# Kernel optimization log

Hardware: AMD Instinct MI355X
Metric: run time of the kernel (lower is better)

## Reference

```python
import jax, jax.numpy as jnp
import numpy as np

EPS = 1e-08

def setup_inputs() -> dict:
    key = jax.random.key(0)
    k1, k2, k3, k4 = jax.random.split(key, 4)
    B, T, D, D_sample = 16, 512, 2048, 4096
    z_hist = jax.random.normal(k1, (B, T, D), dtype=jnp.float32)
    decay_rates = jax.random.normal(k2, (D_sample,), dtype=jnp.float32)
    idx_i = jax.random.randint(k3, (D_sample,), 0, D)
    idx_j = jax.random.randint(k4, (D_sample,), 0, D)
    return {"z_hist": z_hist, "decay_rates": decay_rates, "idx_i": idx_i, "idx_j": idx_j}

def reference(z_hist, decay_rates, idx_i, idx_j):
    B, T, D = z_hist.shape
    r = jax.nn.softplus(decay_rates)                      # [N]
    times = jnp.arange(T, dtype=z_hist.dtype)             # [T]
    # decay[t, n] = exp(-r_n * (T - 1 - t))
    decay = jnp.exp(-r[None, :] * (T - 1 - times)[:, None])  # [T, N]
    z_i = z_hist[:, :, idx_i]                              # [B, T, N]
    z_j = z_hist[:, :, idx_j]                              # [B, T, N]
    num = jnp.einsum('btn,btn,tn->bn', z_i, z_j, decay)    # [B, N]
    den = jnp.sqrt(decay.sum(axis=0) + EPS)                # [N]
    return num / den[None, :]
```

## Files before the change

kernel.cpp:

```cpp
#include <hip/hip_runtime.h>
#include <hip/hip_bf16.h>
#include <math.h>

#define B_   16
#define T_   512
#define D_   2048
#define DS_  4096
#define TCHUNK 4
#define EPS_ 1e-8f


__global__ __launch_bounds__(256) void pre_kernel(const float* __restrict__ decay_rates,
                                                  float* __restrict__ num,
                                                  float* __restrict__ inv_den,
                                                  float* __restrict__ neg_r,
                                                  float* __restrict__ er) {
    int gtid = blockIdx.x * 256 + threadIdx.x;
    num[gtid] = 0.f;
    if (gtid < DS_) {
        float x = decay_rates[gtid];
        float r = (x > 20.f) ? x : log1pf(expf(x));
        float S = expm1f(-r * (float)T_) / expm1f(-r);
        inv_den[gtid] = 1.0f / sqrtf(S + EPS_);
        neg_r[gtid]   = -r;
        er[gtid]      = expf(r);
    }
}

__global__ __launch_bounds__(256, 5) void main_kernel(const float* __restrict__ z,
                                                      const int* __restrict__ idx_i,
                                                      const int* __restrict__ idx_j,
                                                      const float* __restrict__ neg_r,
                                                      const float* __restrict__ er,
                                                      float* __restrict__ num) {
    __shared__ float4 quads[D_];
    const int tc  = blockIdx.x;
    const int b   = blockIdx.y;
    const int tid = threadIdx.x;
    const int t0  = tc * TCHUNK;
    const float* base = z + ((size_t)b * T_ + t0) * D_;

    #pragma unroll
    for (int it = 0; it < D_ / 256; ++it) {
        int c = tid + it * 256;
        quads[c] = make_float4(base[c], base[D_ + c], base[2 * D_ + c], base[3 * D_ + c]);
    }
    __syncthreads();

    const int kbase = (T_ - 1) - t0;

    #pragma unroll 1
    for (int s = 0; s < DS_ / 256; ++s) {
        const int n  = tid + s * 256;
        const int ii = idx_i[n];
        const int jj = idx_j[n];
        const float g = er[n];
        const float w0 = __expf(neg_r[n] * (float)kbase);
        float4 vi = quads[ii];
        float4 vj = quads[jj];
        float p0 = vi.x * vj.x;
        float p1 = vi.y * vj.y;
        float p2 = vi.z * vj.z;
        float p3 = vi.w * vj.w;
        float acc = w0 * (p0 + g * (p1 + g * (p2 + g * p3)));
        atomicAdd(&num[b * DS_ + n], acc);
    }
}

__global__ __launch_bounds__(256) void fin_kernel(const float* __restrict__ num,
                                                  const float* __restrict__ inv_den,
                                                  float* __restrict__ out) {
    int gtid = blockIdx.x * 256 + threadIdx.x;
    out[gtid] = num[gtid] * inv_den[gtid & (DS_ - 1)];
}

extern "C" void kernel_launch(void* const* d_in, const int* in_sizes, int n_in,
                              void* d_out, int out_size, void* d_ws, size_t ws_size,
                              hipStream_t stream) {
    const float* z  = (const float*)d_in[0];
    const float* dr = (const float*)d_in[1];
    const int*   ii = (const int*)d_in[2];
    const int*   jj = (const int*)d_in[3];
    float* out = (float*)d_out;

    float* num     = (float*)d_ws;
    float* inv_den = num + B_ * DS_;
    float* neg_r   = inv_den + DS_;
    float* er      = neg_r + DS_;

    hipLaunchKernelGGL(pre_kernel, dim3((B_ * DS_) / 256), dim3(256), 0, stream,
                       dr, num, inv_den, neg_r, er);
    hipLaunchKernelGGL(main_kernel, dim3(T_ / TCHUNK, B_), dim3(256), 0, stream,
                       z, ii, jj, neg_r, er, num);
    hipLaunchKernelGGL(fin_kernel, dim3((B_ * DS_) / 256), dim3(256), 0, stream,
                       num, inv_den, out);
}
```

Before: 135.4 us.

## Bucket samples by decay horizon and skip negligibly decayed time steps

A new single-block kernel buckets the sampled pairs by how many time steps their decay weight stays above roughly exp(-34.5). It stores per-bucket parameters in sorted order so warps get uniform skip decisions. The main kernel now handles two time chunks per block, keeps accumulators in registers, and updates the weight multiplicatively with a precomputed exp(-4r). It skips pairs whose decay is negligible and issues one atomic per pair per block. This cuts LDS gathers, exp evaluations and atomic traffic. It adds an extra launch and still loads the full z slab in every block.

```diff
diff --git a/kernel.cpp b/kernel.cpp
--- a/kernel.cpp
+++ b/kernel.cpp
@@ -1,70 +1,145 @@
 #include <hip/hip_runtime.h>
-#include <hip/hip_bf16.h>
 #include <math.h>
 
-#define B_   16
-#define T_   512
-#define D_   2048
-#define DS_  4096
+#define B_    16
+#define T_    512
+#define D_    2048
+#define DS_   4096
 #define TCHUNK 4
-#define EPS_ 1e-8f
+#define TCPB   2
+#define TSPLIT (T_ / (TCHUNK * TCPB))
+#define EPS_  1e-8f
+#define CLOG  34.5f
 
+
+__device__ __forceinline__ float softplus_f(float x) {
+    return (x > 20.f) ? x : log1pf(expf(x));
+}
 
 __global__ __launch_bounds__(256) void pre_kernel(const float* __restrict__ decay_rates,
                                                   float* __restrict__ num,
-                                                  float* __restrict__ inv_den,
-                                                  float* __restrict__ neg_r,
-                                                  float* __restrict__ er) {
+                                                  float* __restrict__ inv_den) {
     int gtid = blockIdx.x * 256 + threadIdx.x;
     num[gtid] = 0.f;
     if (gtid < DS_) {
-        float x = decay_rates[gtid];
-        float r = (x > 20.f) ? x : log1pf(expf(x));
+        float r = softplus_f(decay_rates[gtid]);
         float S = expm1f(-r * (float)T_) / expm1f(-r);
         inv_den[gtid] = 1.0f / sqrtf(S + EPS_);
-        neg_r[gtid]   = -r;
-        er[gtid]      = expf(r);
     }
 }
 
-__global__ __launch_bounds__(256, 5) void main_kernel(const float* __restrict__ z,
-                                                      const int* __restrict__ idx_i,
-                                                      const int* __restrict__ idx_j,
-                                                      const float* __restrict__ neg_r,
-                                                      const float* __restrict__ er,
+__global__ __launch_bounds__(1024) void sort_kernel(const float* __restrict__ decay_rates,
+                                                    const int* __restrict__ idx_i,
+                                                    const int* __restrict__ idx_j,
+                                                    float* __restrict__ g_s,
+                                                    float* __restrict__ e4m_s,
+                                                    float* __restrict__ nr_s,
+                                                    int* __restrict__ pair_s,
+                                                    int* __restrict__ nout_s,
+                                                    int* __restrict__ hcap_s) {
+    __shared__ int hist[64];
+    const int tid = threadIdx.x;
+    if (tid < 64) hist[tid] = 0;
+    __syncthreads();
+    #pragma unroll
+    for (int k = 0; k < 4; ++k) {
+        int n = tid + k * 1024;
+        float r = softplus_f(decay_rates[n]);
+        float hf = CLOG / r;
+        int h = (hf >= 511.f) ? 511 : (int)hf;
+        atomicAdd(&hist[h >> 3], 1);
+    }
+    __syncthreads();
+    if (tid == 0) {
+        int run = 0;
+        for (int q = 63; q >= 0; --q) { int c = hist[q]; hist[q] = run; run += c; }
+    }
+    __syncthreads();
+    #pragma unroll
+    for (int k = 0; k < 4; ++k) {
+        int n = tid + k * 1024;
+        float r = softplus_f(decay_rates[n]);
+        float hf = CLOG / r;
+        int h = (hf >= 511.f) ? 511 : (int)hf;
+        int q = h >> 3;
+        int pos = atomicAdd(&hist[q], 1);
+        g_s[pos]    = expf(r);
+        e4m_s[pos]  = expf(-4.f * r);
+        nr_s[pos]   = -r;
+        pair_s[pos] = idx_i[n] | (idx_j[n] << 16);
+        nout_s[pos] = n;
+        hcap_s[pos] = (q << 3) | 7;
+    }
+}
+
+__global__ __launch_bounds__(256, 4) void main_kernel(const float* __restrict__ z,
+                                                      const float* __restrict__ g_s,
+                                                      const float* __restrict__ e4m_s,
+                                                      const float* __restrict__ nr_s,
+                                                      const int* __restrict__ pair_s,
+                                                      const int* __restrict__ nout_s,
+                                                      const int* __restrict__ hcap_s,
                                                       float* __restrict__ num) {
     __shared__ float4 quads[D_];
-    const int tc  = blockIdx.x;
-    const int b   = blockIdx.y;
-    const int tid = threadIdx.x;
-    const int t0  = tc * TCHUNK;
-    const float* base = z + ((size_t)b * T_ + t0) * D_;
+    const int tbase = blockIdx.x * (TCHUNK * TCPB);
+    const int b     = blockIdx.y;
+    const int tid   = threadIdx.x;
 
+    int hb[16];
     #pragma unroll
-    for (int it = 0; it < D_ / 256; ++it) {
-        int c = tid + it * 256;
-        quads[c] = make_float4(base[c], base[D_ + c], base[2 * D_ + c], base[3 * D_ + c]);
+    for (int s = 0; s < 16; ++s)
+        hb[s] = __builtin_amdgcn_readfirstlane(hcap_s[tid + s * 256]);
+
+    const int kbW = 504 - tbase;
+    const int kb1 = 507 - tbase;
+
+    float g[16], w0[16], acc[16];
+    int pair[16];
+    #pragma unroll
+    for (int s = 0; s < 16; ++s) {
+        acc[s] = 0.f;
+        if (hb[s] >= kbW) {
+            int m = tid + s * 256;
+            pair[s] = pair_s[m];
+            g[s]    = g_s[m];
+            w0[s]   = __expf(nr_s[m] * (float)kb1);
+        }
     }
-    __syncthreads();
 
-    const int kbase = (T_ - 1) - t0;
-
+    const float* zb = z + (size_t)b * T_ * D_;
     #pragma unroll 1
-    for (int s = 0; s < DS_ / 256; ++s) {
-        const int n  = tid + s * 256;
-        const int ii = idx_i[n];
-        const int jj = idx_j[n];
-        const float g = er[n];
-        const float w0 = __expf(neg_r[n] * (float)kbase);
-        float4 vi = quads[ii];
-        float4 vj = quads[jj];
-        float p0 = vi.x * vj.x;
-        float p1 = vi.y * vj.y;
-        float p2 = vi.z * vj.z;
-        float p3 = vi.w * vj.w;
-        float acc = w0 * (p0 + g * (p1 + g * (p2 + g * p3)));
-        atomicAdd(&num[b * DS_ + n], acc);
+    for (int c = TCPB - 1; c >= 0; --c) {
+        const int t0 = tbase + c * TCHUNK;
+        const float* base = zb + (size_t)t0 * D_;
+        #pragma unroll
+        for (int it = 0; it < D_ / 256; ++it) {
+            int ci = tid + it * 256;
+            quads[ci] = make_float4(base[ci], base[D_ + ci],
+                                    base[2 * D_ + ci], base[3 * D_ + ci]);
+        }
+        __syncthreads();
+        const int kmin = 508 - t0;
+        #pragma unroll
+        for (int s = 0; s < 16; ++s) {
+            if (hb[s] >= kmin) {
+                int pk = pair[s];
+                float4 vi = quads[pk & 0xFFFF];
+                float4 vj = quads[pk >> 16];
+                float gs = g[s];
+                float h3 = vi.w * vj.w;
+                float h2 = fmaf(h3, gs, vi.z * vj.z);
+                float h1 = fmaf(h2, gs, vi.y * vj.y);
+                float h0 = fmaf(h1, gs, vi.x * vj.x);
+                acc[s] = fmaf(w0[s], h0, acc[s]);
+                if (c > 0) w0[s] *= e4m_s[tid + s * 256];
+            }
+        }
+        __syncthreads();
     }
+    #pragma unroll
+    for (int s = 0; s < 16; ++s)
+        if (hb[s] >= kbW && acc[s] != 0.f)
+            atomicAdd(&num[b * DS_ + nout_s[tid + s * 256]], acc[s]);
 }
 
 __global__ __launch_bounds__(256) void fin_kernel(const float* __restrict__ num,
@@ -85,13 +160,19 @@
 
     float* num     = (float*)d_ws;
     float* inv_den = num + B_ * DS_;
-    float* neg_r   = inv_den + DS_;
-    float* er      = neg_r + DS_;
+    float* g_s     = inv_den + DS_;
+    float* e4m_s   = g_s + DS_;
+    float* nr_s    = e4m_s + DS_;
+    int*   pair_s  = (int*)(nr_s + DS_);
+    int*   nout_s  = pair_s + DS_;
+    int*   hcap_s  = nout_s + DS_;
 
     hipLaunchKernelGGL(pre_kernel, dim3((B_ * DS_) / 256), dim3(256), 0, stream,
-                       dr, num, inv_den, neg_r, er);
-    hipLaunchKernelGGL(main_kernel, dim3(T_ / TCHUNK, B_), dim3(256), 0, stream,
-                       z, ii, jj, neg_r, er, num);
+                       dr, num, inv_den);
+    hipLaunchKernelGGL(sort_kernel, dim3(1), dim3(1024), 0, stream,
+                       dr, ii, jj, g_s, e4m_s, nr_s, pair_s, nout_s, hcap_s);
+    hipLaunchKernelGGL(main_kernel, dim3(TSPLIT, B_), dim3(256), 0, stream,
+                       z, g_s, e4m_s, nr_s, pair_s, nout_s, hcap_s, num);
     hipLaunchKernelGGL(fin_kernel, dim3((B_ * DS_) / 256), dim3(256), 0, stream,
                        num, inv_den, out);
 }
```

After: 150.3 us. 11.0% more time.
